# Optimization experiments

Measured on AMD Instinct MI355X. Metric: run time of the kernel, lower is better.

Reference implementation:

```python
import jax, jax.numpy as jnp
import numpy as np

# ContextualAttention config (matches init_kwargs)
KS, STRIDE, DIL, FUSE_K, SCALE = 3, 1, 1, 3, 10.0
B, C, H, W = 2, 128, 64, 64
L = H * W  # number of background patches (SAME padding, stride 1)


def _same_pad(x, k, s):
    # TF-style SAME padding, identical to the repo's same_padding helper
    _, _, h, w = x.shape
    oh, ow = -(-h // s), -(-w // s)
    ph = max(0, (oh - 1) * s + k - h)
    pw = max(0, (ow - 1) * s + k - w)
    return jnp.pad(x, ((0, 0), (0, 0), (ph // 2, ph - ph // 2), (pw // 2, pw - pw // 2)))


def _patches(x, k, s):
    # extract_image_patches: SAME pad + unfold -> [N, L, C*k*k], (c, kh, kw) ordering
    xp = _same_pad(x, k, s)
    n, c, hp, wp = xp.shape
    oh, ow = (hp - k) // s + 1, (wp - k) // s + 1
    cols = jnp.stack(
        [xp[:, :, i:i + (oh - 1) * s + 1:s, j:j + (ow - 1) * s + 1:s]
         for i in range(k) for j in range(k)], axis=2)  # [N, C, k*k, oh, ow]
    return cols.reshape(n, c * k * k, oh * ow).transpose(0, 2, 1)


def _fuse(scores):
    # diagonal fuse-smoothing: conv the [L_b, L_f] score matrix with eye(k), twice
    # (second pass on the transposed spatial layout), exactly as in the torch code
    bn = scores.shape[0]
    eye = jnp.eye(FUSE_K, dtype=scores.dtype)[None, None]  # [1,1,k,k]
    conv = lambda v: jax.lax.conv_general_dilated(
        v, eye, (1, 1), [(1, 1), (1, 1)],
        dimension_numbers=('NCHW', 'OIHW', 'NCHW'))
    y = conv(scores.reshape(bn, 1, L, L))
    y = y.reshape(bn, H, W, H, W).transpose(0, 2, 1, 4, 3).reshape(bn, 1, L, L)
    y = conv(y)
    y = y.reshape(bn, W, H, W, H).transpose(0, 2, 1, 4, 3)  # back to [b,H,W,H,W]
    return y.reshape(bn, L, H, W)


def setup_inputs() -> dict:
    key = jax.random.key(0)
    kf, kb, km = jax.random.split(key, 3)
    f = jax.random.normal(kf, (B, C, H, W), jnp.float32)
    b = jax.random.normal(kb, (B, C, H, W), jnp.float32)
    mask = (jax.random.uniform(km, (1, 1, H, W)) < 0.05).astype(jnp.float32)
    return {"f": f, "b": b, "mask": mask}


def reference(f, b, mask):
    kernel = 2 * DIL  # raw patch size for aggregation (=2)
    # raw background patches used by the transposed-conv aggregation
    raw_w = _patches(b, kernel, DIL * STRIDE).reshape(B, L, C, kernel, kernel)
    # DIL == 1 => F.interpolate(scale=1.0, nearest) is identity on f/b/mask
    w = _patches(b, KS, STRIDE)      # [B, L, C*9] matching patches
    fp = _patches(f, KS, 1)          # [B, Lf, C*9] foreground patches (SAME pad)
    m = _patches(mask, KS, STRIDE)[0]                    # [L, 9]
    mm = (jnp.mean(m, axis=1) == 0.0).astype(f.dtype)    # [L] 1 = patch usable

    # per-patch L2 normalization (clamped at 1e-4), conv-as-similarity == patch GEMM
    wn = w / jnp.maximum(jnp.sqrt(jnp.sum(w * w, axis=2, keepdims=True)), 1e-4)
    scores = jnp.einsum('bkd,bqd->bkq', wn, fp).reshape(B, L, H, W)
    scores = _fuse(scores)

    mmb = mm[None, :, None, None]
    attn = jax.nn.softmax(scores * mmb * SCALE, axis=1) * mmb  # softmax over L

    # conv_transpose2d(attn, raw_w, stride=1, padding=1) == VALID corr with flipped,
    # IO-swapped 2x2 kernel (k-1-p = 0 padding); per-sample weights -> vmap
    def agg(a, rw):  # a: [L,H,W], rw: [L,C,2,2]
        rhs = jnp.flip(rw, axis=(2, 3)).transpose(1, 0, 2, 3)  # [C, L, 2, 2] OIHW
        return jax.lax.conv_general_dilated(
            a[None], rhs, (1, 1), [(0, 0), (0, 0)],
            dimension_numbers=('NCHW', 'OIHW', 'NCHW'))[0]

    y = jax.vmap(agg)(attn, raw_w) / 4.0       # [B, C, H-1, W-1]
    y = jnp.pad(y, ((0, 0), (0, 0), (0, 1), (0, 1)))  # output_padding = DIL % 2 = 1
    return y
```

## Files before the change

### kernel.cpp

```cpp
#include <hip/hip_runtime.h>

#define L 4096
#define HH 64
#define CC 128
#define BB 2
#define KD 1152

typedef _Float16 f16;
typedef _Float16 f16x8 __attribute__((ext_vector_type(8)));
typedef float f32x4 __attribute__((ext_vector_type(4)));

__device__ __forceinline__ void gl_lds16(const f16* g, f16* l) {
  __builtin_amdgcn_global_load_lds(
      (const __attribute__((address_space(1))) void*)g,
      (__attribute__((address_space(3))) void*)l, 16, 0, 0);
}

__device__ __forceinline__ int sigma_(int j) { return ((j & 63) << 6) | (j >> 6); }

__device__ float fuse9(const f16* __restrict__ Sb, int k, int j) {
  float acc = 0.f;
  int cK = sigma_(k), cQ = sigma_(j);
#pragma unroll
  for (int u = -1; u <= 1; ++u) {
    int a = cK + u, bq = cQ + u;
    if ((unsigned)a < L && (unsigned)bq < L) {
      int r = sigma_(a), c = sigma_(bq);
#pragma unroll
      for (int t = -1; t <= 1; ++t) {
        int rr = r + t, cc = c + t;
        if ((unsigned)rr < L && (unsigned)cc < L) acc += (float)Sb[(size_t)rr * L + cc];
      }
    }
  }
  return acc;
}

__global__ __launch_bounds__(256) void k_prep_patches(
    const float* __restrict__ f, const float* __restrict__ b,
    f16* __restrict__ WN, f16* __restrict__ FP) {
  int wid = threadIdx.x >> 6;
  int lane = threadIdx.x & 63;
  int loc = blockIdx.x * 4 + wid;
  int batch = loc >> 12;
  int k = loc & (L - 1);
  int ky = k >> 6, kx = k & 63;
  const float* bp = b + (size_t)batch * CC * L;
  const float* fp_ = f + (size_t)batch * CC * L;
  float bv[18], fv[18];
  float ss = 0.f;
#pragma unroll
  for (int it = 0; it < 18; ++it) {
    int d = it * 64 + lane;
    int c = d / 9;
    int r = d - c * 9;
    int yy = ky + (r / 3) - 1, xx = kx + (r % 3) - 1;
    bool ok = (yy >= 0 && yy < 64 && xx >= 0 && xx < 64);
    float vb = ok ? bp[(size_t)c * L + yy * 64 + xx] : 0.f;
    float vf = ok ? fp_[(size_t)c * L + yy * 64 + xx] : 0.f;
    bv[it] = vb; fv[it] = vf;
    ss += vb * vb;
  }
#pragma unroll
  for (int m = 32; m >= 1; m >>= 1) ss += __shfl_xor(ss, m, 64);
  float scale = 1.f / fmaxf(sqrtf(ss), 1e-4f);
  f16* wn = WN + (size_t)loc * KD;
  f16* fpo = FP + (size_t)loc * KD;
#pragma unroll
  for (int it = 0; it < 18; ++it) {
    int d = it * 64 + lane;
    wn[d] = (f16)(bv[it] * scale);
    fpo[d] = (f16)(fv[it]);
  }
}

__global__ void k_prep_bm(const float* __restrict__ b, f16* __restrict__ bm) {
  int idx = blockIdx.x * 256 + threadIdx.x;
  int k = idx & (L - 1);
  int c = (idx >> 12) & (CC - 1);
  int bt = idx >> 19;
  int batch = bt & 1;
  int tap = bt >> 1;
  int di = 1 - (tap >> 1), dj = 1 - (tap & 1);
  int ky = k >> 6, kx = k & 63;
  float v = 0.f;
  if (ky + di < 64 && kx + dj < 64)
    v = b[((size_t)batch * CC + c) * L + k + di * 64 + dj];
  bm[idx] = (f16)v;
}

__global__ void k_prep_mm(const float* __restrict__ mask, float* __restrict__ mmv) {
  int k = blockIdx.x * 256 + threadIdx.x;
  if (k >= L) return;
  int ky = k >> 6, kx = k & 63;
  float s = 0.f;
  for (int i = 0; i < 3; ++i)
    for (int j = 0; j < 3; ++j) {
      int yy = ky + i - 1, xx = kx + j - 1;
      if (yy >= 0 && yy < 64 && xx >= 0 && xx < 64) s += mask[yy * 64 + xx];
    }
  mmv[k] = (s == 0.f) ? 1.f : 0.f;
}

__global__ __launch_bounds__(256) void k_gemm_scores(
    const f16* __restrict__ WN, const f16* __restrict__ FP, f16* __restrict__ S) {
  __shared__ f16 As[128 * 64];
  __shared__ f16 Bs[128 * 64];
  int qt = blockIdx.x, kt = blockIdx.y, batch = blockIdx.z;
  int tid = threadIdx.x, wid = tid >> 6, lane = tid & 63;
  int wr = wid >> 1, wc = wid & 1;
  const f16* Abase = WN + ((size_t)batch * L + kt * 128) * KD;
  const f16* Bbase = FP + ((size_t)batch * L + qt * 128) * KD;
  f32x4 acc[4][4] = {};
  int rA = wr * 64 + (lane & 15);
  int rB = wc * 64 + (lane & 15);
  for (int kk = 0; kk < KD; kk += 64) {
    __syncthreads();
#pragma unroll
    for (int i = 0; i < 4; ++i) {
      int chunk = (i * 4 + wid) * 64 + lane;
      int row = chunk >> 3;
      int lg = (lane & 7) ^ (row & 7);
      gl_lds16(Abase + (size_t)row * KD + kk + lg * 8, As + chunk * 8);
      gl_lds16(Bbase + (size_t)row * KD + kk + lg * 8, Bs + chunk * 8);
    }
    __syncthreads();
#pragma unroll
    for (int half = 0; half < 2; ++half) {
      int cb = half * 4 + (lane >> 4);
      f16x8 af[4], bf[4];
#pragma unroll
      for (int m = 0; m < 4; ++m) {
        int row = rA + m * 16;
        af[m] = *(const f16x8*)(As + row * 64 + ((cb ^ (row & 7)) * 8));
      }
#pragma unroll
      for (int n = 0; n < 4; ++n) {
        int row = rB + n * 16;
        bf[n] = *(const f16x8*)(Bs + row * 64 + ((cb ^ (row & 7)) * 8));
      }
#pragma unroll
      for (int m = 0; m < 4; ++m)
#pragma unroll
        for (int n = 0; n < 4; ++n)
          acc[m][n] = __builtin_amdgcn_mfma_f32_16x16x32_f16(af[m], bf[n], acc[m][n], 0, 0, 0);
    }
  }
  f16* Srow = S + (size_t)batch * L * L;
  int kbase = kt * 128 + wr * 64 + (lane >> 4) * 4;
  int qbase = qt * 128 + wc * 64 + (lane & 15);
#pragma unroll
  for (int m = 0; m < 4; ++m)
#pragma unroll
    for (int r = 0; r < 4; ++r) {
      f16* dst = Srow + (size_t)(kbase + m * 16 + r) * L + qbase;
#pragma unroll
      for (int n = 0; n < 4; ++n) dst[n * 16] = (f16)acc[m][n][r];
    }
}

__global__ __launch_bounds__(256) void k_fuse_stats(
    const f16* __restrict__ S, const float* __restrict__ mmv,
    float* __restrict__ T3, float* __restrict__ pm, float* __restrict__ pl) {
  int tid = threadIdx.x;
  if (tid >= 247) return;
  int jc = blockIdx.x, kc = blockIdx.y, batch = blockIdx.z;
  int g = jc * 247 + tid;
  int q0 = 72 + g * 8;
  const f16* Sb = S + (size_t)batch * L * L;
  float* Tb = T3 + (size_t)batch * L * L;
  float m8[8], l8[8];
#pragma unroll
  for (int e = 0; e < 8; ++e) { m8[e] = -3.0e38f; l8[e] = 0.f; }
  int cnt = 0;
  int k0 = kc * 16;
  for (int kk = 0; kk < 16; ++kk) {
    int k = k0 + kk;
    if (mmv[k] == 0.f) { ++cnt; continue; }
    float acc[8] = {0.f, 0.f, 0.f, 0.f, 0.f, 0.f, 0.f, 0.f};
    int cK = sigma_(k);
#pragma unroll
    for (int u = -1; u <= 1; ++u) {
      int a = cK + u;
      if ((unsigned)a >= L) continue;
      int r = sigma_(a);
      const f16* cb = Sb + (size_t)r * L + (q0 + 64 * u);
      {
        f16x8 v = *(const f16x8*)cb;
#pragma unroll
        for (int e = 0; e < 8; ++e) acc[e] += (float)v[e];
      }
      if (r >= 1) {
        const f16* rm = cb - L;
        f16x8 v = *(const f16x8*)rm;
        acc[0] += (float)rm[-1];
#pragma unroll
        for (int e = 1; e < 8; ++e) acc[e] += (float)v[e - 1];
      }
      if (r <= L - 2) {
        const f16* rp = cb + L;
        f16x8 v = *(const f16x8*)rp;
#pragma unroll
        for (int e = 0; e < 7; ++e) acc[e] += (float)v[e + 1];
        acc[7] += (float)rp[8];
      }
    }
#pragma unroll
    for (int e = 0; e < 8; ++e) acc[e] *= 10.f;
    float* trow = Tb + (size_t)k * L + q0;
    *(f32x4*)trow = *(f32x4*)&acc[0];
    *(f32x4*)(trow + 4) = *(f32x4*)&acc[4];
#pragma unroll
    for (int e = 0; e < 8; ++e) {
      float nm = fmaxf(m8[e], acc[e]);
      l8[e] = l8[e] * __expf(m8[e] - nm) + __expf(acc[e] - nm);
      m8[e] = nm;
    }
  }
  float fc = (float)cnt;
  float om[8], ol[8];
#pragma unroll
  for (int e = 0; e < 8; ++e) {
    float nm = fmaxf(m8[e], 0.f);
    ol[e] = l8[e] * __expf(m8[e] - nm) + fc * __expf(-nm);
    om[e] = nm;
  }
  float* pmp = pm + (size_t)kc * (BB * L) + (size_t)batch * L + q0;
  float* plp = pl + (size_t)kc * (BB * L) + (size_t)batch * L + q0;
  *(f32x4*)pmp = *(f32x4*)&om[0]; *(f32x4*)(pmp + 4) = *(f32x4*)&om[4];
  *(f32x4*)plp = *(f32x4*)&ol[0]; *(f32x4*)(plp + 4) = *(f32x4*)&ol[4];
}

__global__ __launch_bounds__(256) void k_fuse_stats_edge(
    const f16* __restrict__ S, const float* __restrict__ mmv,
    float* __restrict__ T3, float* __restrict__ pm, float* __restrict__ pl) {
  int tid = threadIdx.x;
  if (tid >= 144) return;
  int q = (tid < 72) ? tid : (4024 + tid - 72);
  int kc = blockIdx.x, batch = blockIdx.y;
  const f16* Sb = S + (size_t)batch * L * L;
  float* Tb = T3 + (size_t)batch * L * L;
  float m = -3.0e38f, l = 0.f;
  int cnt = 0;
  int k0 = kc * 16;
  for (int kk = 0; kk < 16; ++kk) {
    int k = k0 + kk;
    if (mmv[k] == 0.f) { ++cnt; continue; }
    float logit = 10.f * fuse9(Sb, k, q);
    Tb[(size_t)k * L + q] = logit;
    float nm = fmaxf(m, logit);
    l = l * __expf(m - nm) + __expf(logit - nm);
    m = nm;
  }
  float nm = fmaxf(m, 0.f);
  l = l * __expf(m - nm) + (float)cnt * __expf(-nm);
  pm[(size_t)kc * (BB * L) + (size_t)batch * L + q] = nm;
  pl[(size_t)kc * (BB * L) + (size_t)batch * L + q] = l;
}

__global__ void k_softmax_reduce(const float* __restrict__ pm, const float* __restrict__ pl,
                                 float* __restrict__ Mq, float* __restrict__ invLq) {
  int qi = blockIdx.x * 256 + threadIdx.x;
  if (qi >= BB * L) return;
  float M = -3.0e38f;
  for (int i = 0; i < 256; ++i) M = fmaxf(M, pm[(size_t)i * (BB * L) + qi]);
  float Ls = 0.f;
  for (int i = 0; i < 256; ++i) Ls += pl[(size_t)i * (BB * L) + qi] * __expf(pm[(size_t)i * (BB * L) + qi] - M);
  Mq[qi] = M;
  invLq[qi] = 1.f / Ls;
}

__global__ __launch_bounds__(512) void k_agg(
    const float* __restrict__ T3, const float* __restrict__ mmv,
    const float* __restrict__ Mq, const float* __restrict__ invLq,
    const f16* __restrict__ bm, float* __restrict__ part) {
  __shared__ f16 Asm[512 * 32];
  __shared__ f16 Bt[136 * 40];
  int pt = blockIdx.x, ks = blockIdx.y, batch = blockIdx.z;
  int p0 = pt * 64;
  int tid = threadIdx.x, wid = tid >> 6, lane = tid & 63;
  int wr = wid >> 1, wc = wid & 1;
  const float* Tb = T3 + (size_t)batch * L * L;
  const float* mq0 = Mq + (size_t)batch * L;
  const float* il0 = invLq + (size_t)batch * L;
  f32x4 acc[2][2] = {};
  int kend = ks * 1024 + 1024;
  for (int k0 = ks * 1024; k0 < kend; k0 += 32) {
    __syncthreads();
#pragma unroll
    for (int i = 0; i < 4; ++i) {
      int R = wid * 64 + i * 16 + (lane >> 2);
      int tap = R >> 7, c = R & 127;
      int chl = (lane & 3) ^ ((R >> 1) & 3);
      const f16* g = bm + (((size_t)(tap * 2 + batch) * CC + c) * L) + k0 + chl * 8;
      gl_lds16(g, Asm + R * 32 + (lane & 3) * 8);
    }
    for (int tau = tid; tau < 544; tau += 512) {
      int kk = tau / 17, ch = tau - kk * 17;
      int k = k0 + kk;
      int pbase = p0 + ch * 8;
      f16 v[8];
      if (mmv[k] != 0.f) {
        const float* trow = Tb + (size_t)k * L + pbase;
        if (pbase + 7 < L) {
          f32x4 t0 = *(const f32x4*)trow;
          f32x4 t1 = *(const f32x4*)(trow + 4);
          f32x4 m0 = *(const f32x4*)(mq0 + pbase);
          f32x4 m1 = *(const f32x4*)(mq0 + pbase + 4);
          f32x4 i0 = *(const f32x4*)(il0 + pbase);
          f32x4 i1 = *(const f32x4*)(il0 + pbase + 4);
#pragma unroll
          for (int e = 0; e < 4; ++e) v[e] = (f16)(__expf(t0[e] - m0[e]) * i0[e]);
#pragma unroll
          for (int e = 0; e < 4; ++e) v[4 + e] = (f16)(__expf(t1[e] - m1[e]) * i1[e]);
        } else {
#pragma unroll
          for (int e = 0; e < 8; ++e) {
            int q = pbase + e;
            v[e] = (q < L) ? (f16)(__expf(trow[e] - mq0[q]) * il0[q]) : (f16)0.f;
          }
        }
      } else {
#pragma unroll
        for (int e = 0; e < 8; ++e) v[e] = (f16)0.f;
      }
#pragma unroll
      for (int e = 0; e < 8; ++e) {
        int pp = ch * 8 + e;
        Bt[pp * 40 + (((kk >> 3) ^ ((pp >> 3) & 3)) * 8) + (kk & 7)] = v[e];
      }
    }
    __syncthreads();
#pragma unroll
    for (int tap = 0; tap < 4; ++tap) {
      int dlt = (tap >> 1) * 64 + (tap & 1);
      f16x8 af[2], bf[2];
#pragma unroll
      for (int m = 0; m < 2; ++m) {
        int R = tap * 128 + wr * 32 + m * 16 + (lane & 15);
        int ph = (lane >> 4) ^ ((R >> 1) & 3);
        af[m] = *(const f16x8*)(Asm + R * 32 + ph * 8);
      }
#pragma unroll
      for (int n = 0; n < 2; ++n) {
        int pp = wc * 32 + n * 16 + (lane & 15) + dlt;
        int ph = (lane >> 4) ^ ((pp >> 3) & 3);
        bf[n] = *(const f16x8*)(Bt + pp * 40 + ph * 8);
      }
#pragma unroll
      for (int m = 0; m < 2; ++m)
#pragma unroll
        for (int n = 0; n < 2; ++n)
          acc[m][n] = __builtin_amdgcn_mfma_f32_16x16x32_f16(af[m], bf[n], acc[m][n], 0, 0, 0);
    }
  }
  int cb = wr * 32 + (lane >> 4) * 4;
  int pb = p0 + wc * 32 + (lane & 15);
#pragma unroll
  for (int m = 0; m < 2; ++m)
#pragma unroll
    for (int n = 0; n < 2; ++n)
#pragma unroll
      for (int r = 0; r < 4; ++r) {
        int c = cb + m * 16 + r;
        int p = pb + n * 16;
        part[(((size_t)ks * 2 + batch) * CC + c) * L + p] = acc[m][n][r];
      }
}

__global__ void k_agg_reduce(const float* __restrict__ part, float* __restrict__ out) {
  int idx = blockIdx.x * 256 + threadIdx.x;
  int p = idx & (L - 1);
  float s = 0.f;
#pragma unroll
  for (int ks = 0; ks < 4; ++ks) s += part[(size_t)ks * (2 * CC * L) + idx];
  int u = p >> 6, v = p & 63;
  out[idx] = (u < 63 && v < 63) ? s * 0.25f : 0.f;
}

extern "C" void kernel_launch(void* const* d_in, const int* in_sizes, int n_in,
                              void* d_out, int out_size, void* d_ws, size_t ws_size,
                              hipStream_t stream) {
  const float* f = (const float*)d_in[0];
  const float* b = (const float*)d_in[1];
  const float* mask = (const float*)d_in[2];
  float* out = (float*)d_out;
  char* ws = (char*)d_ws;

  f16* WN    = (f16*)(ws + 0);
  f16* FP    = (f16*)(ws + 18874368);
  float* T3  = (float*)(ws + 0);
  f16* S     = (f16*)(ws + 134217728);
  f16* bm    = (f16*)(ws + 201326592);
  float* part= (float*)(ws + 209715200);
  float* pm  = (float*)(ws + 226492416);
  float* pl  = (float*)(ws + 234881024);
  float* mmv = (float*)(ws + 243269632);
  float* Mq  = (float*)(ws + 243286016);
  float* iLq = (float*)(ws + 243318784);

  k_prep_patches<<<dim3(2048), dim3(256), 0, stream>>>(f, b, WN, FP);
  k_prep_bm<<<dim3(16384), dim3(256), 0, stream>>>(b, bm);
  k_prep_mm<<<dim3(16), dim3(256), 0, stream>>>(mask, mmv);
  k_gemm_scores<<<dim3(32, 32, 2), dim3(256), 0, stream>>>(WN, FP, S);
  k_fuse_stats<<<dim3(2, 256, 2), dim3(256), 0, stream>>>(S, mmv, T3, pm, pl);
  k_fuse_stats_edge<<<dim3(256, 2), dim3(256), 0, stream>>>(S, mmv, T3, pm, pl);
  k_softmax_reduce<<<dim3(32), dim3(256), 0, stream>>>(pm, pl, Mq, iLq);
  k_agg<<<dim3(64, 4, 2), dim3(512), 0, stream>>>(T3, mmv, Mq, iLq, bm, part);
  k_agg_reduce<<<dim3(4096), dim3(256), 0, stream>>>(part, out);
}
```

Measured before the change: 379.9 us.

## Replace materialized im2col patches with implicit shifted-tap GEMM over channel-last inputs

Drops the explicit 9x-expanded f16 patch matrices (WN/FP) and instead repacks b and f into channel-last f16 layout. The score GEMM then builds each K-slice by loading spatially shifted rows per 3x3 tap, using a zero pad buffer at borders. Patch normalization moves to a per-row scale applied in the epilogue, computed from per-pixel sums of squares. The prep_bm and agg_reduce kernels are also vectorized. This removes large prep traffic at the cost of more address logic in the GEMM loads, and the K ordering changes from (c,kh,kw) to (tap,c), so fp16 rounding differs slightly.

```diff
diff --git a/kernel.cpp b/kernel.cpp
--- a/kernel.cpp
+++ b/kernel.cpp
@@ -4,7 +4,6 @@
 #define HH 64
 #define CC 128
 #define BB 2
-#define KD 1152
 
 typedef _Float16 f16;
 typedef _Float16 f16x8 __attribute__((ext_vector_type(8)));
@@ -36,57 +35,80 @@
   return acc;
 }
 
-__global__ __launch_bounds__(256) void k_prep_patches(
-    const float* __restrict__ f, const float* __restrict__ b,
-    f16* __restrict__ WN, f16* __restrict__ FP) {
-  int wid = threadIdx.x >> 6;
-  int lane = threadIdx.x & 63;
-  int loc = blockIdx.x * 4 + wid;
-  int batch = loc >> 12;
-  int k = loc & (L - 1);
+__global__ __launch_bounds__(256) void k_repack(
+    const float* __restrict__ b, const float* __restrict__ f,
+    f16* __restrict__ bT, f16* __restrict__ fT, f16* __restrict__ zp) {
+  __shared__ float tile[128][65];
+  int u0 = blockIdx.x * 64;
+  int z = blockIdx.y;
+  int batch = z >> 1;
+  const float* src = ((z & 1) ? f : b) + (size_t)batch * CC * L;
+  f16* dst = ((z & 1) ? fT : bT) + (size_t)batch * L * CC;
+  int tid = threadIdx.x;
+  if (blockIdx.x == 0 && z == 0 && tid < 32) zp[tid] = (f16)0.f;
+#pragma unroll
+  for (int i = 0; i < 32; ++i) {
+    int idx = i * 256 + tid;
+    int c = idx >> 6, ux = idx & 63;
+    tile[c][ux] = src[(size_t)c * L + u0 + ux];
+  }
+  __syncthreads();
+#pragma unroll
+  for (int j = 0; j < 4; ++j) {
+    int t2 = j * 256 + tid;
+    int u = t2 >> 4, ch = t2 & 15;
+    f16x8 v;
+#pragma unroll
+    for (int e = 0; e < 8; ++e) v[e] = (f16)tile[ch * 8 + e][u];
+    *(f16x8*)(dst + (size_t)(u0 + u) * CC + ch * 8) = v;
+  }
+}
+
+__global__ __launch_bounds__(256) void k_ssq(const float* __restrict__ b, float* __restrict__ ssq) {
+  int u = blockIdx.x * 256 + threadIdx.x;
+  int batch = blockIdx.y;
+  const float* bp = b + (size_t)batch * CC * L + u;
+  float s = 0.f;
+#pragma unroll 4
+  for (int c = 0; c < CC; ++c) { float v = bp[(size_t)c * L]; s += v * v; }
+  ssq[batch * L + u] = s;
+}
+
+__global__ void k_norm(const float* __restrict__ ssq, float* __restrict__ inv_n) {
+  int gi = blockIdx.x * 256 + threadIdx.x;
+  if (gi >= BB * L) return;
+  int batch = gi >> 12, k = gi & (L - 1);
   int ky = k >> 6, kx = k & 63;
-  const float* bp = b + (size_t)batch * CC * L;
-  const float* fp_ = f + (size_t)batch * CC * L;
-  float bv[18], fv[18];
-  float ss = 0.f;
-#pragma unroll
-  for (int it = 0; it < 18; ++it) {
-    int d = it * 64 + lane;
-    int c = d / 9;
-    int r = d - c * 9;
-    int yy = ky + (r / 3) - 1, xx = kx + (r % 3) - 1;
-    bool ok = (yy >= 0 && yy < 64 && xx >= 0 && xx < 64);
-    float vb = ok ? bp[(size_t)c * L + yy * 64 + xx] : 0.f;
-    float vf = ok ? fp_[(size_t)c * L + yy * 64 + xx] : 0.f;
-    bv[it] = vb; fv[it] = vf;
-    ss += vb * vb;
-  }
-#pragma unroll
-  for (int m = 32; m >= 1; m >>= 1) ss += __shfl_xor(ss, m, 64);
-  float scale = 1.f / fmaxf(sqrtf(ss), 1e-4f);
-  f16* wn = WN + (size_t)loc * KD;
-  f16* fpo = FP + (size_t)loc * KD;
-#pragma unroll
-  for (int it = 0; it < 18; ++it) {
-    int d = it * 64 + lane;
-    wn[d] = (f16)(bv[it] * scale);
-    fpo[d] = (f16)(fv[it]);
-  }
-}
-
-__global__ void k_prep_bm(const float* __restrict__ b, f16* __restrict__ bm) {
+  float s = 0.f;
+#pragma unroll
+  for (int dy = -1; dy <= 1; ++dy)
+#pragma unroll
+    for (int dx = -1; dx <= 1; ++dx) {
+      if ((unsigned)(ky + dy) < 64 && (unsigned)(kx + dx) < 64)
+        s += ssq[batch * L + k + dy * 64 + dx];
+    }
+  inv_n[gi] = 1.f / fmaxf(sqrtf(s), 1e-4f);
+}
+
+__global__ __launch_bounds__(256) void k_prep_bm(const float* __restrict__ b, f16* __restrict__ bm) {
   int idx = blockIdx.x * 256 + threadIdx.x;
-  int k = idx & (L - 1);
-  int c = (idx >> 12) & (CC - 1);
-  int bt = idx >> 19;
+  int e8 = idx * 8;
+  int k0 = e8 & (L - 1);
+  int c = (e8 >> 12) & (CC - 1);
+  int bt = e8 >> 19;
   int batch = bt & 1;
   int tap = bt >> 1;
   int di = 1 - (tap >> 1), dj = 1 - (tap & 1);
-  int ky = k >> 6, kx = k & 63;
-  float v = 0.f;
-  if (ky + di < 64 && kx + dj < 64)
-    v = b[((size_t)batch * CC + c) * L + k + di * 64 + dj];
-  bm[idx] = (f16)v;
+  int ky = k0 >> 6, kx0 = k0 & 63;
+  const float* src = b + ((size_t)batch * CC + c) * L + k0 + di * 64 + dj;
+  bool rowok = (ky + di) < 64;
+  f16x8 v;
+#pragma unroll
+  for (int e = 0; e < 8; ++e) {
+    float x = (rowok && (kx0 + e + dj) < 64) ? src[e] : 0.f;
+    v[e] = (f16)x;
+  }
+  *(f16x8*)(bm + (size_t)e8) = v;
 }
 
 __global__ void k_prep_mm(const float* __restrict__ mask, float* __restrict__ mmv) {
@@ -103,31 +125,47 @@
 }
 
 __global__ __launch_bounds__(256) void k_gemm_scores(
-    const f16* __restrict__ WN, const f16* __restrict__ FP, f16* __restrict__ S) {
+    const f16* __restrict__ bT, const f16* __restrict__ fT,
+    const float* __restrict__ inv_n, const f16* __restrict__ zp,
+    f16* __restrict__ S) {
   __shared__ f16 As[128 * 64];
   __shared__ f16 Bs[128 * 64];
   int qt = blockIdx.x, kt = blockIdx.y, batch = blockIdx.z;
   int tid = threadIdx.x, wid = tid >> 6, lane = tid & 63;
   int wr = wid >> 1, wc = wid & 1;
-  const f16* Abase = WN + ((size_t)batch * L + kt * 128) * KD;
-  const f16* Bbase = FP + ((size_t)batch * L + qt * 128) * KD;
+  const f16* A0 = bT + (size_t)batch * L * CC;
+  const f16* B0 = fT + (size_t)batch * L * CC;
   f32x4 acc[4][4] = {};
   int rA = wr * 64 + (lane & 15);
   int rB = wc * 64 + (lane & 15);
-  for (int kk = 0; kk < KD; kk += 64) {
+  for (int t = 0; t < 18; ++t) {
+    int r = t >> 1, half = t & 1;
+    int dy = r / 3 - 1, dx = r - (r / 3) * 3 - 1;
+    int dlt = dy * 64 + dx;
     __syncthreads();
 #pragma unroll
     for (int i = 0; i < 4; ++i) {
       int chunk = (i * 4 + wid) * 64 + lane;
       int row = chunk >> 3;
       int lg = (lane & 7) ^ (row & 7);
-      gl_lds16(Abase + (size_t)row * KD + kk + lg * 8, As + chunk * 8);
-      gl_lds16(Bbase + (size_t)row * KD + kk + lg * 8, Bs + chunk * 8);
+      int off = half * 64 + lg * 8;
+      {
+        int k = kt * 128 + row;
+        bool va = ((unsigned)((k >> 6) + dy) < 64) && ((unsigned)((k & 63) + dx) < 64);
+        const f16* ga = va ? (A0 + (size_t)(k + dlt) * CC + off) : zp;
+        gl_lds16(ga, As + chunk * 8);
+      }
+      {
+        int q = qt * 128 + row;
+        bool vb = ((unsigned)((q >> 6) + dy) < 64) && ((unsigned)((q & 63) + dx) < 64);
+        const f16* gb = vb ? (B0 + (size_t)(q + dlt) * CC + off) : zp;
+        gl_lds16(gb, Bs + chunk * 8);
+      }
     }
     __syncthreads();
 #pragma unroll
-    for (int half = 0; half < 2; ++half) {
-      int cb = half * 4 + (lane >> 4);
+    for (int h2 = 0; h2 < 2; ++h2) {
+      int cb = h2 * 4 + (lane >> 4);
       f16x8 af[4], bf[4];
 #pragma unroll
       for (int m = 0; m < 4; ++m) {
@@ -150,13 +188,15 @@
   int kbase = kt * 128 + wr * 64 + (lane >> 4) * 4;
   int qbase = qt * 128 + wc * 64 + (lane & 15);
 #pragma unroll
-  for (int m = 0; m < 4; ++m)
+  for (int m = 0; m < 4; ++m) {
+    f32x4 invv = *(const f32x4*)(inv_n + (size_t)batch * L + kbase + m * 16);
 #pragma unroll
     for (int r = 0; r < 4; ++r) {
       f16* dst = Srow + (size_t)(kbase + m * 16 + r) * L + qbase;
 #pragma unroll
-      for (int n = 0; n < 4; ++n) dst[n * 16] = (f16)acc[m][n][r];
-    }
+      for (int n = 0; n < 4; ++n) dst[n * 16] = (f16)(acc[m][n][r] * invv[r]);
+    }
+  }
 }
 
 __global__ __launch_bounds__(256) void k_fuse_stats(
@@ -368,14 +408,21 @@
       }
 }
 
-__global__ void k_agg_reduce(const float* __restrict__ part, float* __restrict__ out) {
-  int idx = blockIdx.x * 256 + threadIdx.x;
+__global__ __launch_bounds__(256) void k_agg_reduce(const float* __restrict__ part, float* __restrict__ out) {
+  int idx = (blockIdx.x * 256 + threadIdx.x) * 4;
+  f32x4 s = {0.f, 0.f, 0.f, 0.f};
+#pragma unroll
+  for (int ks = 0; ks < 4; ++ks) {
+    f32x4 v = *(const f32x4*)(part + (size_t)ks * (2 * CC * L) + idx);
+#pragma unroll
+    for (int e = 0; e < 4; ++e) s[e] += v[e];
+  }
   int p = idx & (L - 1);
-  float s = 0.f;
-#pragma unroll
-  for (int ks = 0; ks < 4; ++ks) s += part[(size_t)ks * (2 * CC * L) + idx];
-  int u = p >> 6, v = p & 63;
-  out[idx] = (u < 63 && v < 63) ? s * 0.25f : 0.f;
+  int u = p >> 6, vv = p & 63;
+  f32x4 o;
+#pragma unroll
+  for (int e = 0; e < 4; ++e) o[e] = (u < 63 && (vv + e) < 63) ? s[e] * 0.25f : 0.f;
+  *(f32x4*)(out + idx) = o;
 }
 
 extern "C" void kernel_launch(void* const* d_in, const int* in_sizes, int n_in,
@@ -387,8 +434,6 @@
   float* out = (float*)d_out;
   char* ws = (char*)d_ws;
 
-  f16* WN    = (f16*)(ws + 0);
-  f16* FP    = (f16*)(ws + 18874368);
   float* T3  = (float*)(ws + 0);
   f16* S     = (f16*)(ws + 134217728);
   f16* bm    = (f16*)(ws + 201326592);
@@ -398,14 +443,21 @@
   float* mmv = (float*)(ws + 243269632);
   float* Mq  = (float*)(ws + 243286016);
   float* iLq = (float*)(ws + 243318784);
-
-  k_prep_patches<<<dim3(2048), dim3(256), 0, stream>>>(f, b, WN, FP);
-  k_prep_bm<<<dim3(16384), dim3(256), 0, stream>>>(b, bm);
+  f16* bT    = (f16*)(ws + 243351552);
+  f16* fT    = (f16*)(ws + 245448704);
+  float* ssq = (float*)(ws + 247545856);
+  float* invn= (float*)(ws + 247578624);
+  f16* zp    = (f16*)(ws + 247611392);
+
+  k_repack<<<dim3(64, 4), dim3(256), 0, stream>>>(b, f, bT, fT, zp);
+  k_ssq<<<dim3(16, 2), dim3(256), 0, stream>>>(b, ssq);
+  k_norm<<<dim3(32), dim3(256), 0, stream>>>(ssq, invn);
+  k_prep_bm<<<dim3(2048), dim3(256), 0, stream>>>(b, bm);
   k_prep_mm<<<dim3(16), dim3(256), 0, stream>>>(mask, mmv);
-  k_gemm_scores<<<dim3(32, 32, 2), dim3(256), 0, stream>>>(WN, FP, S);
+  k_gemm_scores<<<dim3(32, 32, 2), dim3(256), 0, stream>>>(bT, fT, invn, zp, S);
   k_fuse_stats<<<dim3(2, 256, 2), dim3(256), 0, stream>>>(S, mmv, T3, pm, pl);
   k_fuse_stats_edge<<<dim3(256, 2), dim3(256), 0, stream>>>(S, mmv, T3, pm, pl);
   k_softmax_reduce<<<dim3(32), dim3(256), 0, stream>>>(pm, pl, Mq, iLq);
   k_agg<<<dim3(64, 4, 2), dim3(512), 0, stream>>>(T3, mmv, Mq, iLq, bm, part);
-  k_agg_reduce<<<dim3(4096), dim3(256), 0, stream>>>(part, out);
-}
+  k_agg_reduce<<<dim3(1024), dim3(256), 0, stream>>>(part, out);
+}
```

Result: no change. 377.2 us (-0.7%).
